# Optimization experiments

Measured on AMD Instinct MI355X. Metric: run time of the kernel, lower is better.

Reference implementation:

```python
import jax, jax.numpy as jnp
import numpy as np

TOP_K = 8  # num_experts_per_tok


def setup_inputs() -> dict:
    key = jax.random.key(0)
    k1, k2 = jax.random.split(key)
    hidden_states = jax.random.normal(k1, (4, 4096, 2048), dtype=jnp.float32)
    weight = jax.random.normal(k2, (128, 2048), dtype=jnp.float32) * 0.02
    return {"hidden_states": hidden_states, "weight": weight}


def reference(hidden_states, weight):
    B, S, H = hidden_states.shape
    x = hidden_states.reshape(-1, H).astype(jnp.float32)        # [T, H], T = B*S
    logits = jnp.einsum("th,eh->te", x, weight.astype(jnp.float32))  # [T, E]
    scores = jax.nn.softmax(logits, axis=-1)                    # float32 softmax
    topk_weight, topk_idx = jax.lax.top_k(scores, TOP_K)        # [T, K]
    # norm_topk_prob=True: renormalize selected probabilities
    topk_weight = topk_weight / jnp.sum(topk_weight, axis=-1, keepdims=True)
    return topk_idx, topk_weight
```

## Files before the change

kernel.cpp:

```cpp
#include <hip/hip_runtime.h>
#include <math.h>

#define T_TOKENS 16384
#define HDIM     2048
#define NEXP     128
#define TOPK     8

#define BK    128
#define NCH   (HDIM / BK)
#define TM    32

#define F16_MIN_NORM    6.1035156e-05f
#define SPLIT_SCALE     4096.0f
#define INV_SPLIT_SCALE 2.44140625e-04f

typedef __attribute__((ext_vector_type(8))) _Float16 f16x8;
typedef __attribute__((ext_vector_type(4))) float    f32x4;

#define LGKM0()   asm volatile("s_waitcnt lgkmcnt(0)" ::: "memory")

__device__ __forceinline__ void f16split(float f, _Float16& hi, _Float16& lo) {
    _Float16 h = (_Float16)f;
    float back = (float)h;
    if (fabsf(f) < F16_MIN_NORM) { h = (_Float16)0.f; back = 0.f; }
    lo = (_Float16)((f - back) * SPLIT_SCALE);
    hi = h;
}

__device__ __forceinline__ int swz(int b) {
    return b ^ (((b >> 8) & 3) << 4) ^ (((b >> 11) & 1) << 6);
}

__global__ __launch_bounds__(256) void pack_w(const float* __restrict__ w,
                                              unsigned short* __restrict__ wp1,
                                              unsigned short* __restrict__ wp2) {
    int p = blockIdx.x * 256 + threadIdx.x;
    int lane = p & 63, nt = (p >> 6) & 7, kk = p >> 9;
    int col = lane & 15, quad = lane >> 4;
    const float* src = w + (size_t)(nt * 16 + col) * HDIM + kk * 32 + quad * 8;
    unsigned short h[8], l[8];
#pragma unroll
    for (int j = 0; j < 8; ++j) {
        _Float16 hh, ll;
        f16split(src[j], hh, ll);
        union { _Float16 x; unsigned short u; } ch, cl;
        ch.x = hh; cl.x = ll;
        h[j] = ch.u; l[j] = cl.u;
    }
    *(uint4*)(wp1 + (size_t)p * 8) = *(const uint4*)h;
    *(uint4*)(wp2 + (size_t)p * 8) = *(const uint4*)l;
}

struct ARegs { f32x4 v[4]; };
struct BRegs { f16x8 v[16]; };

__global__ __launch_bounds__(256, 2) void moe_gate(const float* __restrict__ x,
                                                   const unsigned short* __restrict__ wp1,
                                                   const unsigned short* __restrict__ wp2,
                                                   float* __restrict__ out_idx,
                                                   float* __restrict__ out_w) {
    __shared__ __align__(16) unsigned char smem[32768];
    float* epil = (float*)smem;

    const int tid  = threadIdx.x;
    const int lane = tid & 63;
    const int wv   = tid >> 6;
    const int col  = lane & 15;
    const int quad = lane >> 4;
    const long tok0 = (long)blockIdx.x * TM;

    const int srow = tid >> 3, skseg = tid & 7;
    const float* xgs = x + (tok0 + srow) * (long)HDIM + skseg * 8;
    const int g0 = (skseg >> 2) * 2 + (srow >> 4);
    const int g1 = ((skseg + 8) >> 2) * 2 + (srow >> 4);
    const int adst0 = swz(g0 * 1024 + (skseg & 3) * 256 + (srow & 15) * 16);
    const int adst1 = swz(g1 * 1024 + (skseg & 3) * 256 + (srow & 15) * 16);

    f32x4 acc[2][2], accc[2][2];
#pragma unroll
    for (int m = 0; m < 2; ++m)
#pragma unroll
        for (int j = 0; j < 2; ++j) { acc[m][j] = (f32x4){0,0,0,0}; accc[m][j] = (f32x4){0,0,0,0}; }

    auto loadA = [&](int ch, ARegs& A) {
        const float* p = xgs + ch * BK;
        A.v[0] = *(const f32x4*)(p);
        A.v[1] = *(const f32x4*)(p + 4);
        A.v[2] = *(const f32x4*)(p + 64);
        A.v[3] = *(const f32x4*)(p + 68);
    };
    auto splitWriteA = [&](const ARegs& A, int b) {
        unsigned short h0[8], l0[8], h1[8], l1[8];
#pragma unroll
        for (int j = 0; j < 8; ++j) {
            _Float16 hh, ll;
            f16split(j < 4 ? A.v[0][j] : A.v[1][j - 4], hh, ll);
            union { _Float16 x; unsigned short u; } ch_, cl_;
            ch_.x = hh; cl_.x = ll;
            h0[j] = ch_.u; l0[j] = cl_.u;
            f16split(j < 4 ? A.v[2][j] : A.v[3][j - 4], hh, ll);
            ch_.x = hh; cl_.x = ll;
            h1[j] = ch_.u; l1[j] = cl_.u;
        }
        unsigned char* base = smem + b * 16384;
        *(uint4*)(base + adst0)        = *(const uint4*)h0;
        *(uint4*)(base + adst1)        = *(const uint4*)h1;
        *(uint4*)(base + 8192 + adst0) = *(const uint4*)l0;
        *(uint4*)(base + 8192 + adst1) = *(const uint4*)l1;
    };
    auto loadB = [&](int ch, BRegs& B) {
#pragma unroll
        for (int kk = 0; kk < 4; ++kk)
#pragma unroll
            for (int j = 0; j < 2; ++j) {
                const size_t o = (size_t)(ch * 4 + kk) * 4096
                               + (size_t)(wv * 2 + j) * 512 + (size_t)lane * 8;
                B.v[(kk * 2 + j) * 2 + 0] = *(const f16x8*)(wp1 + o);
                B.v[(kk * 2 + j) * 2 + 1] = *(const f16x8*)(wp2 + o);
            }
    };
    auto mfmaStep = [&](int b, const BRegs& B) {
        const unsigned char* base = smem + b * 16384;
#pragma unroll
        for (int kk = 0; kk < 4; ++kk) {
            f16x8 af1v[2], af2v[2];
#pragma unroll
            for (int m = 0; m < 2; ++m) {
                const int bo = swz((kk * 2 + m) * 1024 + lane * 16);
                af1v[m] = *(const f16x8*)(base + bo);
                af2v[m] = *(const f16x8*)(base + 8192 + bo);
            }
#pragma unroll
            for (int j = 0; j < 2; ++j) {
                f16x8 bf1 = B.v[(kk * 2 + j) * 2 + 0];
                f16x8 bf2 = B.v[(kk * 2 + j) * 2 + 1];
#pragma unroll
                for (int m = 0; m < 2; ++m) {
                    acc[m][j]  = __builtin_amdgcn_mfma_f32_16x16x32_f16(af1v[m], bf1, acc[m][j],  0, 0, 0);
                    accc[m][j] = __builtin_amdgcn_mfma_f32_16x16x32_f16(af1v[m], bf2, accc[m][j], 0, 0, 0);
                    accc[m][j] = __builtin_amdgcn_mfma_f32_16x16x32_f16(af2v[m], bf1, accc[m][j], 0, 0, 0);
                }
            }
        }
    };

    ARegs AP, AQ;
    BRegs B0, B1;

    loadA(0, AP);
    loadB(0, B0);
    loadB(1, B1);
    splitWriteA(AP, 0);
    loadA(1, AQ);
    LGKM0();
    __builtin_amdgcn_s_barrier();

    for (int ch = 0; ch < NCH - 2; ch += 2) {
        loadA(ch + 2, AP);
        splitWriteA(AQ, 1);
        mfmaStep(0, B0);
        loadB(ch + 2, B0);
        LGKM0();
        __builtin_amdgcn_s_barrier();

        loadA(ch + 3, AQ);
        splitWriteA(AP, 0);
        mfmaStep(1, B1);
        loadB(ch + 3, B1);
        LGKM0();
        __builtin_amdgcn_s_barrier();
    }
    splitWriteA(AQ, 1);
    mfmaStep(0, B0);
    LGKM0();
    __builtin_amdgcn_s_barrier();
    mfmaStep(1, B1);
    __syncthreads();

#pragma unroll
    for (int m = 0; m < 2; ++m)
#pragma unroll
        for (int j = 0; j < 2; ++j)
#pragma unroll
            for (int r = 0; r < 4; ++r)
                epil[(m * 16 + quad * 4 + r) * 132 + (wv * 2 + j) * 16 + col] =
                    acc[m][j][r] + accc[m][j][r] * INV_SPLIT_SCALE;
    __syncthreads();

    for (int i = 0; i < 8; ++i) {
        const int t = wv * 8 + i;
        float2 p = *(const float2*)(epil + t * 132 + 2 * lane);
        float v0 = p.x, v1 = p.y;
        const int i0 = 2 * lane, i1 = 2 * lane + 1;

        float topv[TOPK];
        int topi[TOPK];
#pragma unroll
        for (int s = 0; s < TOPK; ++s) {
            float mv = (v0 >= v1) ? v0 : v1;
            int   mi = (v0 >= v1) ? i0 : i1;
#pragma unroll
            for (int off = 32; off >= 1; off >>= 1) {
                float ov = __shfl_xor(mv, off);
                int   oi = __shfl_xor(mi, off);
                if (ov > mv || (ov == mv && oi < mi)) { mv = ov; mi = oi; }
            }
            topv[s] = mv; topi[s] = mi;
            if (i0 == mi) v0 = -INFINITY;
            if (i1 == mi) v1 = -INFINITY;
        }

        const float m = topv[0];
        float sum = 0.f;
#pragma unroll
        for (int s = 0; s < TOPK; ++s) sum += expf(topv[s] - m);
        const float inv = 1.f / sum;

        float myv = topv[0]; int myi = topi[0];
#pragma unroll
        for (int s = 1; s < TOPK; ++s)
            if (lane == s) { myv = topv[s]; myi = topi[s]; }

        if (lane < TOPK) {
            long tok = tok0 + t;
            out_idx[tok * TOPK + lane] = (float)myi;
            out_w[tok * TOPK + lane]   = expf(myv - m) * inv;
        }
    }
}

extern "C" void kernel_launch(void* const* d_in, const int* in_sizes, int n_in,
                              void* d_out, int out_size, void* d_ws, size_t ws_size,
                              hipStream_t stream) {
    const float* x = (const float*)d_in[0];
    const float* w = (const float*)d_in[1];
    float* out = (float*)d_out;

    unsigned short* wp1 = (unsigned short*)d_ws;
    unsigned short* wp2 = wp1 + (size_t)NEXP * HDIM;

    pack_w<<<(64 * 8 * 64) / 256, 256, 0, stream>>>(w, wp1, wp2);
    moe_gate<<<T_TOKENS / TM, 256, 0, stream>>>(x, wp1, wp2, out, out + (size_t)T_TOKENS * TOPK);
}
```

Before: 234.3 us.

## Split work across 8 waves per block, one expert tile per wave

Doubles the block to 512 threads so each of 8 waves owns one 16-expert column tile instead of two. Per-thread A loads, B fragments and accumulators are halved, and the top-k epilogue handles 4 tokens per wave instead of 8. The goal is lower register pressure and more waves in flight to hide global-memory latency, at the cost of more barrier participants and the same per-block A-tile traffic spread thinner.

```diff
diff --git a/kernel.cpp b/kernel.cpp
--- a/kernel.cpp
+++ b/kernel.cpp
@@ -51,10 +51,10 @@
     *(uint4*)(wp2 + (size_t)p * 8) = *(const uint4*)l;
 }
 
-struct ARegs { f32x4 v[4]; };
-struct BRegs { f16x8 v[16]; };
-
-__global__ __launch_bounds__(256, 2) void moe_gate(const float* __restrict__ x,
+struct ARegs { f32x4 v[2]; };
+struct BRegs { f16x8 v[8]; };
+
+__global__ __launch_bounds__(512, 4) void moe_gate(const float* __restrict__ x,
                                                    const unsigned short* __restrict__ wp1,
                                                    const unsigned short* __restrict__ wp2,
                                                    float* __restrict__ out_idx,
@@ -69,55 +69,41 @@
     const int quad = lane >> 4;
     const long tok0 = (long)blockIdx.x * TM;
 
-    const int srow = tid >> 3, skseg = tid & 7;
+    const int srow = tid >> 4, skseg = tid & 15;
     const float* xgs = x + (tok0 + srow) * (long)HDIM + skseg * 8;
     const int g0 = (skseg >> 2) * 2 + (srow >> 4);
-    const int g1 = ((skseg + 8) >> 2) * 2 + (srow >> 4);
-    const int adst0 = swz(g0 * 1024 + (skseg & 3) * 256 + (srow & 15) * 16);
-    const int adst1 = swz(g1 * 1024 + (skseg & 3) * 256 + (srow & 15) * 16);
-
-    f32x4 acc[2][2], accc[2][2];
-#pragma unroll
-    for (int m = 0; m < 2; ++m)
-#pragma unroll
-        for (int j = 0; j < 2; ++j) { acc[m][j] = (f32x4){0,0,0,0}; accc[m][j] = (f32x4){0,0,0,0}; }
+    const int adst = swz(g0 * 1024 + (skseg & 3) * 256 + (srow & 15) * 16);
+
+    f32x4 acc[2], accc[2];
+#pragma unroll
+    for (int m = 0; m < 2; ++m) { acc[m] = (f32x4){0,0,0,0}; accc[m] = (f32x4){0,0,0,0}; }
 
     auto loadA = [&](int ch, ARegs& A) {
         const float* p = xgs + ch * BK;
         A.v[0] = *(const f32x4*)(p);
         A.v[1] = *(const f32x4*)(p + 4);
-        A.v[2] = *(const f32x4*)(p + 64);
-        A.v[3] = *(const f32x4*)(p + 68);
     };
     auto splitWriteA = [&](const ARegs& A, int b) {
-        unsigned short h0[8], l0[8], h1[8], l1[8];
+        unsigned short h[8], l[8];
 #pragma unroll
         for (int j = 0; j < 8; ++j) {
             _Float16 hh, ll;
             f16split(j < 4 ? A.v[0][j] : A.v[1][j - 4], hh, ll);
             union { _Float16 x; unsigned short u; } ch_, cl_;
             ch_.x = hh; cl_.x = ll;
-            h0[j] = ch_.u; l0[j] = cl_.u;
-            f16split(j < 4 ? A.v[2][j] : A.v[3][j - 4], hh, ll);
-            ch_.x = hh; cl_.x = ll;
-            h1[j] = ch_.u; l1[j] = cl_.u;
+            h[j] = ch_.u; l[j] = cl_.u;
         }
         unsigned char* base = smem + b * 16384;
-        *(uint4*)(base + adst0)        = *(const uint4*)h0;
-        *(uint4*)(base + adst1)        = *(const uint4*)h1;
-        *(uint4*)(base + 8192 + adst0) = *(const uint4*)l0;
-        *(uint4*)(base + 8192 + adst1) = *(const uint4*)l1;
+        *(uint4*)(base + adst)        = *(const uint4*)h;
+        *(uint4*)(base + 8192 + adst) = *(const uint4*)l;
     };
     auto loadB = [&](int ch, BRegs& B) {
 #pragma unroll
-        for (int kk = 0; kk < 4; ++kk)
-#pragma unroll
-            for (int j = 0; j < 2; ++j) {
-                const size_t o = (size_t)(ch * 4 + kk) * 4096
-                               + (size_t)(wv * 2 + j) * 512 + (size_t)lane * 8;
-                B.v[(kk * 2 + j) * 2 + 0] = *(const f16x8*)(wp1 + o);
-                B.v[(kk * 2 + j) * 2 + 1] = *(const f16x8*)(wp2 + o);
-            }
+        for (int kk = 0; kk < 4; ++kk) {
+            const size_t o = (size_t)(ch * 4 + kk) * 4096 + (size_t)wv * 512 + (size_t)lane * 8;
+            B.v[kk * 2 + 0] = *(const f16x8*)(wp1 + o);
+            B.v[kk * 2 + 1] = *(const f16x8*)(wp2 + o);
+        }
     };
     auto mfmaStep = [&](int b, const BRegs& B) {
         const unsigned char* base = smem + b * 16384;
@@ -130,16 +116,13 @@
                 af1v[m] = *(const f16x8*)(base + bo);
                 af2v[m] = *(const f16x8*)(base + 8192 + bo);
             }
-#pragma unroll
-            for (int j = 0; j < 2; ++j) {
-                f16x8 bf1 = B.v[(kk * 2 + j) * 2 + 0];
-                f16x8 bf2 = B.v[(kk * 2 + j) * 2 + 1];
-#pragma unroll
-                for (int m = 0; m < 2; ++m) {
-                    acc[m][j]  = __builtin_amdgcn_mfma_f32_16x16x32_f16(af1v[m], bf1, acc[m][j],  0, 0, 0);
-                    accc[m][j] = __builtin_amdgcn_mfma_f32_16x16x32_f16(af1v[m], bf2, accc[m][j], 0, 0, 0);
-                    accc[m][j] = __builtin_amdgcn_mfma_f32_16x16x32_f16(af2v[m], bf1, accc[m][j], 0, 0, 0);
-                }
+            f16x8 bf1 = B.v[kk * 2 + 0];
+            f16x8 bf2 = B.v[kk * 2 + 1];
+#pragma unroll
+            for (int m = 0; m < 2; ++m) {
+                acc[m]  = __builtin_amdgcn_mfma_f32_16x16x32_f16(af1v[m], bf1, acc[m],  0, 0, 0);
+                accc[m] = __builtin_amdgcn_mfma_f32_16x16x32_f16(af1v[m], bf2, accc[m], 0, 0, 0);
+                accc[m] = __builtin_amdgcn_mfma_f32_16x16x32_f16(af2v[m], bf1, accc[m], 0, 0, 0);
             }
         }
     };
@@ -180,15 +163,13 @@
 #pragma unroll
     for (int m = 0; m < 2; ++m)
 #pragma unroll
-        for (int j = 0; j < 2; ++j)
-#pragma unroll
-            for (int r = 0; r < 4; ++r)
-                epil[(m * 16 + quad * 4 + r) * 132 + (wv * 2 + j) * 16 + col] =
-                    acc[m][j][r] + accc[m][j][r] * INV_SPLIT_SCALE;
+        for (int r = 0; r < 4; ++r)
+            epil[(m * 16 + quad * 4 + r) * 132 + wv * 16 + col] =
+                acc[m][r] + accc[m][r] * INV_SPLIT_SCALE;
     __syncthreads();
 
-    for (int i = 0; i < 8; ++i) {
-        const int t = wv * 8 + i;
+    for (int i = 0; i < 4; ++i) {
+        const int t = wv * 4 + i;
         float2 p = *(const float2*)(epil + t * 132 + 2 * lane);
         float v0 = p.x, v1 = p.y;
         const int i0 = 2 * lane, i1 = 2 * lane + 1;
@@ -240,5 +221,5 @@
     unsigned short* wp2 = wp1 + (size_t)NEXP * HDIM;
 
     pack_w<<<(64 * 8 * 64) / 256, 256, 0, stream>>>(w, wp1, wp2);
-    moe_gate<<<T_TOKENS / TM, 256, 0, stream>>>(x, wp1, wp2, out, out + (size_t)T_TOKENS * TOPK);
-}
+    moe_gate<<<T_TOKENS / TM, 512, 0, stream>>>(x, wp1, wp2, out, out + (size_t)T_TOKENS * TOPK);
+}
```

Result: faster. 228.0 us (-2.7%).
